# Optimization experiments

Hardware: AMD Instinct MI355X
Metric: run time of the kernel (lower is better)

The kernel has to match this reference:

```python
import jax, jax.numpy as jnp
import numpy as np

N = 32768; D = 384; P = 3; CORR_D = 2 * 49 * P * P  # 882
G_KK = 4096; G_JK = 512
EPS = 1e-3  # LayerNorm eps in the torch module

FLOAT_NAMES = ("net","inp","corr","corr_w1","corr_b1","corr_w2","corr_b2","corr_ln_g","corr_ln_b","corr_w3","corr_b3","norm_g","norm_b","c1_w1","c1_b1","c1_w2","c1_b2","c2_w1","c2_b1","c2_w2","c2_b2","kk_fw","kk_fb","kk_gw","kk_gb","kk_hw","kk_hb","ij_fw","ij_fb","ij_gw","ij_gb","ij_hw","ij_hb","g_ln1_g","g_ln1_b","g1_gw","g1_gb","g1_r1w","g1_r1b","g1_r2w","g1_r2b","g_ln2_g","g_ln2_b","g2_gw","g2_gb","g2_r1w","g2_r1b","g2_r2w","g2_r2b","d_w","d_b","w_w","w_b")

def _ln(x, g, b):
    m = jnp.mean(x, -1, keepdims=True)
    v = jnp.mean((x - m) ** 2, -1, keepdims=True)
    return (x - m) * jax.lax.rsqrt(v + EPS) * g + b

def _mlp2(x, w1, b1, w2, b2):
    return jax.nn.relu(x @ w1 + b1) @ w2 + b2

def _gated_residual(x, gw, gb, r1w, r1b, r2w, r2b):
    gate = jax.nn.sigmoid(x @ gw + gb)
    res = jax.nn.relu(x @ r1w + r1b) @ r2w + r2b
    return x + gate * res

def _soft_agg(x, jx, fw, fb, gw, gb, hw, hb, num_groups):
    # x: [N, D]; jx: [N] group ids -> group-wise softmax weighted sum
    logits = x @ gw + gb
    feats = x @ fw + fb
    gmax = jax.ops.segment_max(logits, jx, num_segments=num_groups)
    e = jnp.exp(logits - gmax[jx])
    den = jax.ops.segment_sum(e, jx, num_segments=num_groups)
    w = e / (den[jx] + 1e-12)
    y = jax.ops.segment_sum(feats * w, jx, num_segments=num_groups)
    return (y @ hw + hb)[jx]

def _forward(p, nix, njx, ukk, ujk):
    # corr encoder MLP
    h = jax.nn.relu(p["corr"] @ p["corr_w1"] + p["corr_b1"]) @ p["corr_w2"] + p["corr_b2"]
    h = jax.nn.relu(_ln(h, p["corr_ln_g"], p["corr_ln_b"])) @ p["corr_w3"] + p["corr_b3"]
    net = p["net"] + p["inp"] + h
    net = _ln(net, p["norm_g"], p["norm_b"])
    mask_ix = (nix >= 0).astype(net.dtype).reshape(1, -1, 1)
    mask_jx = (njx >= 0).astype(net.dtype).reshape(1, -1, 1)
    net = net + _mlp2(mask_ix * net[:, nix], p["c1_w1"], p["c1_b1"], p["c1_w2"], p["c1_b2"])
    net = net + _mlp2(mask_jx * net[:, njx], p["c2_w1"], p["c2_b1"], p["c2_w2"], p["c2_b2"])
    net = net + _soft_agg(net[0], ukk, p["kk_fw"], p["kk_fb"], p["kk_gw"], p["kk_gb"], p["kk_hw"], p["kk_hb"], G_KK)[None]
    net = net + _soft_agg(net[0], ujk, p["ij_fw"], p["ij_fb"], p["ij_gw"], p["ij_gb"], p["ij_hw"], p["ij_hb"], G_JK)[None]
    net = _ln(net, p["g_ln1_g"], p["g_ln1_b"])
    net = _gated_residual(net, p["g1_gw"], p["g1_gb"], p["g1_r1w"], p["g1_r1b"], p["g1_r2w"], p["g1_r2b"])
    net = _ln(net, p["g_ln2_g"], p["g_ln2_b"])
    net = _gated_residual(net, p["g2_gw"], p["g2_gb"], p["g2_r1w"], p["g2_r1b"], p["g2_r2w"], p["g2_r2b"])
    r = jax.nn.relu(net)
    d = r @ p["d_w"] + p["d_b"]               # GradClip is identity in forward
    w = jax.nn.sigmoid(r @ p["w_w"] + p["w_b"])
    return net, d, w

def setup_inputs() -> dict:
    key = jax.random.key(0)
    it = iter(jax.random.split(key, 64))
    def pr(*shape):
        return jax.random.normal(next(it), shape, dtype=jnp.float32) * 0.02
    z = lambda *s: jnp.zeros(s, jnp.float32)
    o = lambda *s: jnp.ones(s, jnp.float32)
    inp = {
        "net": jax.random.normal(next(it), (1, N, D), dtype=jnp.float32),
        "inp": jax.random.normal(next(it), (1, N, D), dtype=jnp.float32),
        "corr": jax.random.normal(next(it), (1, N, CORR_D), dtype=jnp.float32),
        "nix": jax.random.randint(next(it), (N,), 0, N),
        "njx": jax.random.randint(next(it), (N,), 0, N),
        "ukk": jax.random.randint(next(it), (N,), 0, G_KK),
        "ujk": jax.random.randint(next(it), (N,), 0, G_JK),
        "corr_w1": pr(CORR_D, D), "corr_b1": z(D), "corr_w2": pr(D, D), "corr_b2": z(D),
        "corr_ln_g": o(D), "corr_ln_b": z(D), "corr_w3": pr(D, D), "corr_b3": z(D),
        "norm_g": o(D), "norm_b": z(D),
        "c1_w1": pr(D, D), "c1_b1": z(D), "c1_w2": pr(D, D), "c1_b2": z(D),
        "c2_w1": pr(D, D), "c2_b1": z(D), "c2_w2": pr(D, D), "c2_b2": z(D),
        "kk_fw": pr(D, D), "kk_fb": z(D), "kk_gw": pr(D, D), "kk_gb": z(D), "kk_hw": pr(D, D), "kk_hb": z(D),
        "ij_fw": pr(D, D), "ij_fb": z(D), "ij_gw": pr(D, D), "ij_gb": z(D), "ij_hw": pr(D, D), "ij_hb": z(D),
        "g_ln1_g": o(D), "g_ln1_b": z(D),
        "g1_gw": pr(D, D), "g1_gb": z(D), "g1_r1w": pr(D, D), "g1_r1b": z(D), "g1_r2w": pr(D, D), "g1_r2b": z(D),
        "g_ln2_g": o(D), "g_ln2_b": z(D),
        "g2_gw": pr(D, D), "g2_gb": z(D), "g2_r1w": pr(D, D), "g2_r1b": z(D), "g2_r2w": pr(D, D), "g2_r2b": z(D),
        "d_w": pr(D, 2), "d_b": z(2), "w_w": pr(D, 2), "w_b": z(2),
    }
    return inp

def reference(net, inp, corr, corr_w1, corr_b1, corr_w2, corr_b2, corr_ln_g, corr_ln_b, corr_w3, corr_b3, norm_g, norm_b, c1_w1, c1_b1, c1_w2, c1_b2, c2_w1, c2_b1, c2_w2, c2_b2, kk_fw, kk_fb, kk_gw, kk_gb, kk_hw, kk_hb, ij_fw, ij_fb, ij_gw, ij_gb, ij_hw, ij_hb, g_ln1_g, g_ln1_b, g1_gw, g1_gb, g1_r1w, g1_r1b, g1_r2w, g1_r2b, g_ln2_g, g_ln2_b, g2_gw, g2_gb, g2_r1w, g2_r1b, g2_r2w, g2_r2b, d_w, d_b, w_w, w_b, nix, njx, ukk, ujk):
    loc = locals()
    fl = {k: loc[k] for k in FLOAT_NAMES}
    return _forward(fl, nix, njx, ukk, ujk)
```

## Files before the change

### kernel.cpp

```cpp
#include <hip/hip_runtime.h>
#include <hip/hip_bf16.h>
#include <math.h>

#define NR 32768
#define DD 384
#define CDM 882
#define CDMP 896

typedef float f4 __attribute__((ext_vector_type(4)));
typedef float f32x4 __attribute__((ext_vector_type(4)));
typedef __bf16 bf16x8 __attribute__((ext_vector_type(8)));

__device__ inline f4 ld4(const float* p) { f4 v; __builtin_memcpy(&v, p, 16); return v; }
__device__ inline void st4(float* p, f4 v) { __builtin_memcpy(p, &v, 16); }
__device__ inline bf16x8 ld8h(const __bf16* p) { bf16x8 v; __builtin_memcpy(&v, p, 16); return v; }
__device__ inline void st8h(__bf16* p, bf16x8 v) { __builtin_memcpy(p, &v, 16); }

__device__ inline void gl_lds16(const void* g, void* l) {
  __builtin_amdgcn_global_load_lds(
      (const __attribute__((address_space(1))) void*)g,
      (__attribute__((address_space(3))) void*)l, 16, 0, 0);
}

__device__ inline float gred16(float v) {
#pragma unroll
  for (int o = 1; o < 16; o <<= 1) v += __shfl_xor(v, o, 64);
  return v;
}

__global__ __launch_bounds__(256) void corr2bf16_k(const float* __restrict__ src,
                                                   __bf16* __restrict__ dst) {
  int i = blockIdx.x * 256 + threadIdx.x;
  int row = i / 112, c8 = (i - row * 112) * 8;
  const float* sp = src + (size_t)row * CDM + c8;
  bf16x8 h;
  if (c8 + 8 <= CDM) {
#pragma unroll
    for (int e = 0; e < 8; ++e) h[e] = (__bf16)sp[e];
  } else {
#pragma unroll
    for (int e = 0; e < 8; ++e) h[e] = (c8 + e < CDM) ? (__bf16)sp[e] : (__bf16)0.f;
  }
  st8h(dst + (size_t)row * CDMP + c8, h);
}

struct WPtrs { const float* w[19]; };

__global__ __launch_bounds__(256) void trans_all_k(WPtrs P, __bf16* __restrict__ dst) {
  int wi = blockIdx.y;
  const float* W = P.w[wi];
  int i = blockIdx.x * 256 + threadIdx.x;
  if (wi < 18) {
    if (i >= DD * DD) return;
    int n = i / DD, k = i - n * DD;
    dst[(size_t)wi * DD * DD + i] = (__bf16)W[(size_t)k * DD + n];
  } else {
    if (i >= DD * CDMP) return;
    int n = i / CDMP, k = i - n * CDMP;
    dst[(size_t)18 * DD * DD + i] = (k < CDM) ? (__bf16)W[(size_t)k * DD + n] : (__bf16)0.f;
  }
}

struct GP {
  const void* A; const __bf16* WT; const float* bias; __bf16* OUT;
  const __bf16* XRES; const __bf16* GIN;
  const float* p0; const float* p1; const float* p2; const float* p3;
  float* fout; const float* net32; const float* inp32;
  const int* idx; const __bf16* zpage; int M; int K;
};

template <int EPI, int AFP32>
__global__ __launch_bounds__(512, 1) void gemm_k(GP gp) {
  __shared__ __align__(16) __bf16 sm[2 * 32768];
  const int t = threadIdx.x;
  const int w = t >> 6, lane = t & 63;
  const int m0 = blockIdx.x * 128;
  const int fr = lane & 15, fq = lane >> 4;
  const int wr = (w >> 2) * 64, wc = (w & 3) * 96;
  const int K = gp.K;

  const __bf16* aptr[2];
  int aadv[2];
  const __bf16* bptr[6];
#pragma unroll
  for (int j = 0; j < 2; ++j) {
    int rloc = w * 16 + j * 8 + (lane >> 3);
    int cch = (lane & 7) ^ (rloc & 7);
    if constexpr (!AFP32) {
      int ar = gp.idx ? gp.idx[m0 + rloc] : (m0 + rloc);
      if (ar >= 0) { aptr[j] = (const __bf16*)gp.A + (size_t)ar * K + cch * 8; aadv[j] = 64; }
      else { aptr[j] = gp.zpage; aadv[j] = 0; }
    }
  }
#pragma unroll
  for (int j = 0; j < 6; ++j) {
    int rloc = w * 48 + j * 8 + (lane >> 3);
    int cch = (lane & 7) ^ (rloc & 7);
    bptr[j] = gp.WT + (size_t)rloc * K + cch * 8;
  }
  const float* Af = (const float*)gp.A;
  const int NT = K >> 6;

  f32x4 acc[4][6];
#pragma unroll
  for (int a = 0; a < 4; ++a)
#pragma unroll
    for (int b = 0; b < 6; ++b)
#pragma unroll
      for (int j = 0; j < 4; ++j) acc[a][b][j] = 0.f;

  auto stageG = [&](int buf) {
    __bf16* As = sm + buf * 32768;
    __bf16* Bs = As + 8192;
#pragma unroll
    for (int j = 0; j < 2; ++j) {
      gl_lds16(aptr[j], &As[(w * 16 + j * 8) * 64]);
      aptr[j] += aadv[j];
    }
#pragma unroll
    for (int j = 0; j < 6; ++j) {
      gl_lds16(bptr[j], &Bs[(w * 48 + j * 8) * 64]);
      bptr[j] += 64;
    }
  };

  auto stageF = [&](int k0) {
    __bf16* As = sm;
    __bf16* Bs = sm + 8192;
#pragma unroll
    for (int j = 0; j < 2; ++j) {
      int rr = (t >> 3) + 64 * j;
      int cc = t & 7;
      const float* ap = Af + (size_t)(m0 + rr) * K + k0 + cc * 8;
      f4 v0 = ld4(ap), v1 = ld4(ap + 4);
      bf16x8 h;
#pragma unroll
      for (int e = 0; e < 4; ++e) { h[e] = (__bf16)v0[e]; h[4 + e] = (__bf16)v1[e]; }
      *reinterpret_cast<bf16x8*>(&As[rr * 64 + ((cc ^ (rr & 7)) << 3)]) = h;
    }
#pragma unroll
    for (int j = 0; j < 6; ++j) {
      gl_lds16(bptr[j], &Bs[(w * 48 + j * 8) * 64]);
      bptr[j] += 64;
    }
  };

  auto compute = [&](int buf) {
    const __bf16* As = sm + buf * 32768;
    const __bf16* Bs = As + 8192;
#pragma unroll
    for (int kk2 = 0; kk2 < 2; ++kk2) {
      bf16x8 af[4];
      bf16x8 bv[6];
#pragma unroll
      for (int mi = 0; mi < 4; ++mi) {
        int rr = wr + mi * 16 + fr;
        af[mi] = *reinterpret_cast<const bf16x8*>(
            &As[rr * 64 + (((fq + kk2 * 4) ^ (rr & 7)) << 3)]);
      }
#pragma unroll
      for (int ni = 0; ni < 6; ++ni) {
        int rr = wc + ni * 16 + fr;
        bv[ni] = *reinterpret_cast<const bf16x8*>(
            &Bs[rr * 64 + (((fq + kk2 * 4) ^ (rr & 7)) << 3)]);
      }
#pragma unroll
      for (int mi = 0; mi < 4; ++mi)
#pragma unroll
        for (int ni = 0; ni < 6; ++ni)
          acc[mi][ni] = __builtin_amdgcn_mfma_f32_16x16x32_bf16(af[mi], bv[ni],
                                                                acc[mi][ni], 0, 0, 0);
    }
  };

  if constexpr (AFP32) {
    for (int tt = 0; tt < NT; ++tt) {
      if (tt) __syncthreads();
      stageF(tt << 6);
      __syncthreads();
      compute(0);
    }
  } else {
    stageG(0);
    int buf = 0;
    for (int tt = 0; tt < NT; ++tt) {
      if (tt + 1 < NT) {
        stageG(buf ^ 1);
        asm volatile("s_waitcnt vmcnt(8)" ::: "memory");
      } else {
        asm volatile("s_waitcnt vmcnt(0)" ::: "memory");
      }
      __builtin_amdgcn_s_barrier();
      __builtin_amdgcn_sched_barrier(0);
      compute(buf);
      __builtin_amdgcn_s_barrier();
      __builtin_amdgcn_sched_barrier(0);
      buf ^= 1;
    }
  }

  const int nw = w & 3;
  float bcol[6];
#pragma unroll
  for (int ni = 0; ni < 6; ++ni) bcol[ni] = gp.bias[wc + ni * 16 + fr];
#pragma unroll
  for (int mi = 0; mi < 4; ++mi)
#pragma unroll
    for (int ni = 0; ni < 6; ++ni)
#pragma unroll
      for (int j = 0; j < 4; ++j) acc[mi][ni][j] += bcol[ni];

  if constexpr (EPI <= 2) {
#pragma unroll
    for (int mi = 0; mi < 4; ++mi)
#pragma unroll
      for (int ni = 0; ni < 6; ++ni) {
        int col = wc + ni * 16 + fr;
#pragma unroll
        for (int j = 0; j < 4; ++j) {
          int row = m0 + wr + mi * 16 + fq * 4 + j;
          size_t o = (size_t)row * DD + col;
          float v = acc[mi][ni][j];
          if constexpr (EPI == 0) gp.OUT[o] = (__bf16)v;
          else if constexpr (EPI == 1) gp.OUT[o] = (__bf16)fmaxf(v, 0.f);
          else gp.OUT[o] = (__bf16)((float)gp.OUT[o] + v);
        }
      }
  } else {
    if constexpr (EPI == 5) {
#pragma unroll
      for (int mi = 0; mi < 4; ++mi)
#pragma unroll
        for (int ni = 0; ni < 6; ++ni) {
          int col = wc + ni * 16 + fr;
#pragma unroll
          for (int j = 0; j < 4; ++j) {
            int row = m0 + wr + mi * 16 + fq * 4 + j;
            size_t o = (size_t)row * DD + col;
            acc[mi][ni][j] += gp.net32[o] + gp.inp32[o];
          }
        }
    }
    if constexpr (EPI == 6 || EPI == 7) {
#pragma unroll
      for (int mi = 0; mi < 4; ++mi)
#pragma unroll
        for (int ni = 0; ni < 6; ++ni) {
          int col = wc + ni * 16 + fr;
#pragma unroll
          for (int j = 0; j < 4; ++j) {
            int row = m0 + wr + mi * 16 + fq * 4 + j;
            size_t o = (size_t)row * DD + col;
            float gl = (float)gp.GIN[o];
            float sg = 1.f / (1.f + expf(-gl));
            acc[mi][ni][j] = (float)gp.XRES[o] + sg * acc[mi][ni][j];
          }
        }
    }
    __syncthreads();
    if constexpr (EPI != 7) {
      float s1[4][4], s2[4][4];
#pragma unroll
      for (int mi = 0; mi < 4; ++mi)
#pragma unroll
        for (int j = 0; j < 4; ++j) { s1[mi][j] = 0.f; s2[mi][j] = 0.f; }
#pragma unroll
      for (int mi = 0; mi < 4; ++mi)
#pragma unroll
        for (int ni = 0; ni < 6; ++ni)
#pragma unroll
          for (int j = 0; j < 4; ++j) {
            float v = acc[mi][ni][j];
            s1[mi][j] += v;
            s2[mi][j] += v * v;
          }
#pragma unroll
      for (int o = 1; o < 16; o <<= 1)
#pragma unroll
        for (int mi = 0; mi < 4; ++mi)
#pragma unroll
          for (int j = 0; j < 4; ++j) {
            s1[mi][j] += __shfl_xor(s1[mi][j], o, 64);
            s2[mi][j] += __shfl_xor(s2[mi][j], o, 64);
          }
      float* lsum = (float*)sm;
      float* lsq = lsum + 512;
      if (fr == 0) {
#pragma unroll
        for (int mi = 0; mi < 4; ++mi)
#pragma unroll
          for (int j = 0; j < 4; ++j) {
            int rr = wr + mi * 16 + fq * 4 + j;
            lsum[rr * 4 + nw] = s1[mi][j];
            lsq[rr * 4 + nw] = s2[mi][j];
          }
      }
      __syncthreads();
      float mn[4][4], rs[4][4];
#pragma unroll
      for (int mi = 0; mi < 4; ++mi)
#pragma unroll
        for (int j = 0; j < 4; ++j) {
          int rr = wr + mi * 16 + fq * 4 + j;
          float S1 = lsum[rr * 4] + lsum[rr * 4 + 1] + lsum[rr * 4 + 2] + lsum[rr * 4 + 3];
          float S2 = lsq[rr * 4] + lsq[rr * 4 + 1] + lsq[rr * 4 + 2] + lsq[rr * 4 + 3];
          float m = S1 * (1.f / 384.f);
          float va = S2 * (1.f / 384.f) - m * m;
          mn[mi][j] = m;
          rs[mi][j] = rsqrtf(va + 1e-3f);
        }
#pragma unroll
      for (int ni = 0; ni < 6; ++ni) {
        int col = wc + ni * 16 + fr;
        float gg = gp.p0[col], bb = gp.p1[col];
#pragma unroll
        for (int mi = 0; mi < 4; ++mi)
#pragma unroll
          for (int j = 0; j < 4; ++j) {
            int row = m0 + wr + mi * 16 + fq * 4 + j;
            float y = (acc[mi][ni][j] - mn[mi][j]) * rs[mi][j] * gg + bb;
            if constexpr (EPI == 4) y = fmaxf(y, 0.f);
            gp.OUT[(size_t)row * DD + col] = (__bf16)y;
          }
      }
    } else {
      float c0[6], c1[6], c2[6], c3[6];
#pragma unroll
      for (int ni = 0; ni < 6; ++ni) {
        int col = wc + ni * 16 + fr;
        c0[ni] = gp.p0[2 * col];
        c1[ni] = gp.p0[2 * col + 1];
        c2[ni] = gp.p2[2 * col];
        c3[ni] = gp.p2[2 * col + 1];
      }
      float dt[4][4][4];
#pragma unroll
      for (int mi = 0; mi < 4; ++mi)
#pragma unroll
        for (int j = 0; j < 4; ++j)
#pragma unroll
          for (int q = 0; q < 4; ++q) dt[mi][j][q] = 0.f;
#pragma unroll
      for (int mi = 0; mi < 4; ++mi)
#pragma unroll
        for (int ni = 0; ni < 6; ++ni) {
          int col = wc + ni * 16 + fr;
#pragma unroll
          for (int j = 0; j < 4; ++j) {
            int row = m0 + wr + mi * 16 + fq * 4 + j;
            float v = acc[mi][ni][j];
            gp.fout[(size_t)row * DD + col] = v;
            float r = fmaxf(v, 0.f);
            dt[mi][j][0] += r * c0[ni];
            dt[mi][j][1] += r * c1[ni];
            dt[mi][j][2] += r * c2[ni];
            dt[mi][j][3] += r * c3[ni];
          }
        }
#pragma unroll
      for (int o = 1; o < 16; o <<= 1)
#pragma unroll
        for (int mi = 0; mi < 4; ++mi)
#pragma unroll
          for (int j = 0; j < 4; ++j)
#pragma unroll
            for (int q = 0; q < 4; ++q)
              dt[mi][j][q] += __shfl_xor(dt[mi][j][q], o, 64);
      float* lt = (float*)sm;
      if (fr == 0) {
#pragma unroll
        for (int mi = 0; mi < 4; ++mi)
#pragma unroll
          for (int j = 0; j < 4; ++j) {
            int rr = wr + mi * 16 + fq * 4 + j;
#pragma unroll
            for (int q = 0; q < 4; ++q) lt[(rr * 4 + nw) * 4 + q] = dt[mi][j][q];
          }
      }
      __syncthreads();
      if (nw == 0 && fr == 0) {
        float* fd = gp.fout + (size_t)NR * DD;
        float* fw = fd + (size_t)NR * 2;
#pragma unroll
        for (int mi = 0; mi < 4; ++mi)
#pragma unroll
          for (int j = 0; j < 4; ++j) {
            int rr = wr + mi * 16 + fq * 4 + j;
            int row = m0 + rr;
            float T[4];
#pragma unroll
            for (int q = 0; q < 4; ++q)
              T[q] = lt[(rr * 4 + 0) * 4 + q] + lt[(rr * 4 + 1) * 4 + q] +
                     lt[(rr * 4 + 2) * 4 + q] + lt[(rr * 4 + 3) * 4 + q];
            fd[2 * row] = T[0] + gp.p1[0];
            fd[2 * row + 1] = T[1] + gp.p1[1];
            fw[2 * row] = 1.f / (1.f + expf(-(T[2] + gp.p3[0])));
            fw[2 * row + 1] = 1.f / (1.f + expf(-(T[3] + gp.p3[1])));
          }
      }
    }
  }
}

__global__ __launch_bounds__(256) void ln_ag_k(const __bf16* __restrict__ X,
                                               const __bf16* __restrict__ z,
                                               const int* __restrict__ gid,
                                               const float* __restrict__ g,
                                               const float* __restrict__ b,
                                               __bf16* __restrict__ out) {
  int w = threadIdx.x >> 6, lane = threadIdx.x & 63;
  int s = lane & 15, qq = lane >> 4;
  int row = blockIdx.x * 16 + w * 4 + qq;
  int gr = gid[row];
  size_t base = (size_t)row * DD;
  size_t zbase = (size_t)gr * DD;
  float v[24];
#pragma unroll
  for (int i = 0; i < 3; ++i) {
    int col = (s + 16 * i) * 8;
    bf16x8 h = ld8h(X + base + col);
    bf16x8 zz = ld8h(z + zbase + col);
#pragma unroll
    for (int e = 0; e < 8; ++e) v[i * 8 + e] = (float)h[e] + (float)zz[e];
  }
  float sm = 0.f;
#pragma unroll
  for (int i = 0; i < 24; ++i) sm += v[i];
  sm = gred16(sm);
  float mean = sm * (1.f / 384.f);
  float qs = 0.f;
#pragma unroll
  for (int i = 0; i < 24; ++i) { float d = v[i] - mean; qs += d * d; }
  qs = gred16(qs);
  float rs = rsqrtf(qs * (1.f / 384.f) + 1e-3f);
#pragma unroll
  for (int i = 0; i < 3; ++i) {
    int col = (s + 16 * i) * 8;
    f4 g0 = ld4(g + col), g1 = ld4(g + col + 4);
    f4 b0 = ld4(b + col), b1 = ld4(b + col + 4);
    bf16x8 o;
#pragma unroll
    for (int e = 0; e < 4; ++e) {
      o[e] = (__bf16)((v[i * 8 + e] - mean) * rs * g0[e] + b0[e]);
      o[4 + e] = (__bf16)((v[i * 8 + 4 + e] - mean) * rs * g1[e] + b1[e]);
    }
    st8h(out + base + col, o);
  }
}

__global__ __launch_bounds__(256) void hist2_k(const int* __restrict__ ukk,
                                               const int* __restrict__ ujk,
                                               int* __restrict__ ckk,
                                               int* __restrict__ cij) {
  int i = blockIdx.x * 256 + threadIdx.x;
  atomicAdd(&ckk[ukk[i]], 1);
  atomicAdd(&cij[ujk[i]], 1);
}

__device__ inline void scan_body(const int* cnt, int* off, int* curb, int G, int* ls) {
  int t = threadIdx.x;
  int per = G / 256;
  int base = t * per;
  int s = 0;
  for (int i = 0; i < per; ++i) s += cnt[base + i];
  ls[t] = s;
  __syncthreads();
  for (int o = 1; o < 256; o <<= 1) {
    int v = (t >= o) ? ls[t - o] : 0;
    __syncthreads();
    ls[t] += v;
    __syncthreads();
  }
  int run = (t == 0) ? 0 : ls[t - 1];
  for (int i = 0; i < per; ++i) {
    off[base + i] = run;
    run += cnt[base + i];
    curb[base + i] = 0;
  }
  if (t == 255) off[G] = run;
}

__global__ __launch_bounds__(256) void scan2_k(const int* ckk, int* okk, int* qkk,
                                               const int* cij, int* oij, int* qij) {
  __shared__ int ls[256];
  if (blockIdx.x == 0) scan_body(ckk, okk, qkk, 4096, ls);
  else scan_body(cij, oij, qij, 512, ls);
}

__global__ __launch_bounds__(256) void scatter2_k(const int* __restrict__ ukk,
                                                  const int* __restrict__ ujk,
                                                  const int* __restrict__ okk,
                                                  int* __restrict__ qkk,
                                                  int* __restrict__ rkk,
                                                  const int* __restrict__ oij,
                                                  int* __restrict__ qij,
                                                  int* __restrict__ rij) {
  int i = blockIdx.x * 256 + threadIdx.x;
  int g1 = ukk[i];
  rkk[okk[g1] + atomicAdd(&qkk[g1], 1)] = i;
  int g2 = ujk[i];
  rij[oij[g2] + atomicAdd(&qij[g2], 1)] = i;
}

__global__ __launch_bounds__(384) void segagg_k(const __bf16* __restrict__ L,
                                                const __bf16* __restrict__ Ft,
                                                const int* __restrict__ rows,
                                                const int* __restrict__ off,
                                                float* __restrict__ yb) {
  int g = blockIdx.x;
  int c = threadIdx.x;
  int s = off[g], e = off[g + 1];
  float mx = -3.0e38f;
  for (int p = s; p < e; ++p) {
    int r = rows[p];
    mx = fmaxf(mx, (float)L[(size_t)r * DD + c]);
  }
  float num = 0.f, den = 0.f;
  for (int p = s; p < e; ++p) {
    int r = rows[p];
    float lv = (float)L[(size_t)r * DD + c];
    float fv = (float)Ft[(size_t)r * DD + c];
    float ev = expf(lv - mx);
    den += ev;
    num += fv * ev;
  }
  yb[(size_t)g * DD + c] = num / (den + 1e-12f);
}

__global__ __launch_bounds__(256) void addgather_k(__bf16* __restrict__ X,
                                                   const __bf16* __restrict__ z,
                                                   const int* __restrict__ gid) {
  int i = blockIdx.x * 256 + threadIdx.x;
  int row = i / 48, c = (i - row * 48) * 8;
  int g = gid[row];
  size_t lo = (size_t)row * DD + c;
  bf16x8 a = ld8h(X + lo);
  bf16x8 zz = ld8h(z + (size_t)g * DD + c);
  bf16x8 o;
#pragma unroll
  for (int e = 0; e < 8; ++e) o[e] = (__bf16)((float)a[e] + (float)zz[e]);
  st8h(X + lo, o);
}

extern "C" void kernel_launch(void* const* d_in, const int* in_sizes, int n_in,
                              void* d_out, int out_size, void* d_ws, size_t ws_size,
                              hipStream_t stream) {
  const float* in_net = (const float*)d_in[0];
  const float* in_inp = (const float*)d_in[1];
  const float* in_corr = (const float*)d_in[2];
  const int* nix = (const int*)d_in[3];
  const int* njx = (const int*)d_in[4];
  const int* ukk = (const int*)d_in[5];
  const int* ujk = (const int*)d_in[6];
  auto F = [&](int i) { return (const float*)d_in[i]; };

  constexpr size_t MiB = 1024 * 1024;
  constexpr size_t SZ_ACT = (size_t)NR * DD * 2;
  char* ws = (char*)d_ws;
  __bf16* Xc = (__bf16*)(ws);
  __bf16* T2b = (__bf16*)(ws);
  __bf16* Fb = (__bf16*)(ws + SZ_ACT);
  __bf16* zb = (__bf16*)(ws + 2 * SZ_ACT);
  float* yb = (float*)(ws + 2 * SZ_ACT + 3 * MiB);
  __bf16* T1b = (__bf16*)(ws + 60 * MiB);
  char* p = ws + 84 * MiB;
  int* rows_kk = (int*)p; p += (size_t)NR * 4;
  int* rows_ij = (int*)p; p += (size_t)NR * 4;
  int* off_kk = (int*)p; p += 8192 * 4;
  int* off_ij = (int*)p; p += 1024 * 4;
  int* cnt_kk = (int*)p; p += 4096 * 4;
  int* cnt_ij = (int*)p; p += 512 * 4;
  int* curb_kk = (int*)p; p += 4096 * 4;
  int* curb_ij = (int*)p; p += 512 * 4;
  __bf16* wt_all = (__bf16*)p; p += (size_t)18 * DD * DD * 2;
  __bf16* wt_corr1 = (__bf16*)p; p += (size_t)DD * CDMP * 2;
  __bf16* zpage = (__bf16*)p;

  const int widx[18] = {17, 19, 21, 23, 25, 27, 29, 31, 33, 35, 39, 41, 43, 47, 49, 51, 9, 13};
  WPtrs P;
  for (int i = 0; i < 18; ++i) P.w[i] = F(widx[i]);
  P.w[18] = F(7);
  auto WTp = [&](int i) { return wt_all + (size_t)i * DD * DD; };

  hipMemsetAsync(zpage, 0, 256, stream);
  hipMemsetAsync(cnt_kk, 0, 4096 * 4, stream);
  hipMemsetAsync(cnt_ij, 0, 512 * 4, stream);
  trans_all_k<<<dim3(1344, 19), 256, 0, stream>>>(P, wt_all);
  corr2bf16_k<<<NR * 112 / 256, 256, 0, stream>>>(in_corr, Xc);
  hist2_k<<<NR / 256, 256, 0, stream>>>(ukk, ujk, cnt_kk, cnt_ij);
  scan2_k<<<2, 256, 0, stream>>>(cnt_kk, off_kk, curb_kk, cnt_ij, off_ij, curb_ij);
  scatter2_k<<<NR / 256, 256, 0, stream>>>(ukk, ujk, off_kk, curb_kk, rows_kk,
                                           off_ij, curb_ij, rows_ij);

  auto G = [&](int epi, const void* A, const __bf16* WT, const float* bias,
               __bf16* OUT, const __bf16* XRES, const __bf16* GIN,
               const float* p0, const float* p1, const float* p2, const float* p3,
               float* fout, const float* n32, const float* i32,
               const int* idx, int M, int K) {
    GP gp{A, WT, bias, OUT, XRES, GIN, p0, p1, p2, p3, fout, n32, i32, idx, zpage, M, K};
    dim3 g(M / 128), b(512);
    switch (epi) {
      case 0: gemm_k<0, 0><<<g, b, 0, stream>>>(gp); break;
      case 1: gemm_k<1, 0><<<g, b, 0, stream>>>(gp); break;
      case 2: gemm_k<2, 0><<<g, b, 0, stream>>>(gp); break;
      case 4: gemm_k<4, 0><<<g, b, 0, stream>>>(gp); break;
      case 5: gemm_k<5, 0><<<g, b, 0, stream>>>(gp); break;
      case 6: gemm_k<6, 0><<<g, b, 0, stream>>>(gp); break;
      case 7: gemm_k<7, 0><<<g, b, 0, stream>>>(gp); break;
      case 8: gemm_k<0, 1><<<g, b, 0, stream>>>(gp); break;
    }
  };
  auto GS = [&](int epi, const void* A, const __bf16* WT, const float* bias,
                __bf16* OUT, const int* idx, int M, int K) {
    G(epi, A, WT, bias, OUT, nullptr, nullptr, nullptr, nullptr, nullptr, nullptr,
      nullptr, nullptr, nullptr, idx, M, K);
  };

  const int SEGB = NR * 48 / 256;

  GS(1, Xc, wt_corr1, F(8), T1b, nullptr, NR, CDMP);
  G(4, T1b, WTp(16), F(10), T2b, nullptr, nullptr, F(11), F(12), nullptr, nullptr,
    nullptr, nullptr, nullptr, nullptr, NR, DD);
  G(5, T2b, WTp(17), F(14), T1b, nullptr, nullptr, F(15), F(16), nullptr, nullptr,
    nullptr, in_net, in_inp, nullptr, NR, DD);
  GS(1, T1b, WTp(0), F(18), T2b, nix, NR, DD);
  GS(2, T2b, WTp(1), F(20), T1b, nullptr, NR, DD);
  GS(1, T1b, WTp(2), F(22), T2b, njx, NR, DD);
  GS(2, T2b, WTp(3), F(24), T1b, nullptr, NR, DD);
  GS(0, T1b, WTp(5), F(28), T2b, nullptr, NR, DD);
  GS(0, T1b, WTp(4), F(26), Fb, nullptr, NR, DD);
  segagg_k<<<4096, 384, 0, stream>>>(T2b, Fb, rows_kk, off_kk, yb);
  GS(8, yb, WTp(6), F(30), zb, nullptr, 4096, DD);
  addgather_k<<<SEGB, 256, 0, stream>>>(T1b, zb, ukk);
  GS(0, T1b, WTp(8), F(34), T2b, nullptr, NR, DD);
  GS(0, T1b, WTp(7), F(32), Fb, nullptr, NR, DD);
  segagg_k<<<512, 384, 0, stream>>>(T2b, Fb, rows_ij, off_ij, yb);
  GS(8, yb, WTp(9), F(36), zb, nullptr, 512, DD);
  ln_ag_k<<<NR / 16, 256, 0, stream>>>(T1b, zb, ujk, F(37), F(38), T2b);
  GS(0, T2b, WTp(10), F(40), Fb, nullptr, NR, DD);
  GS(1, T2b, WTp(11), F(42), T1b, nullptr, NR, DD);
  G(6, T1b, WTp(12), F(44), T2b, T2b, Fb, F(45), F(46), nullptr, nullptr,
    nullptr, nullptr, nullptr, nullptr, NR, DD);
  GS(0, T2b, WTp(13), F(48), Fb, nullptr, NR, DD);
  GS(1, T2b, WTp(14), F(50), T1b, nullptr, NR, DD);
  G(7, T1b, WTp(15), F(52), nullptr, T2b, Fb, F(53), F(54), F(55), F(56),
    (float*)d_out, nullptr, nullptr, nullptr, NR, DD);
}
```

Measured before the change: 604.5 us.

## Fuse corr bf16 conversion into GEMM and merge shared-input GEMM pairs

Removes the standalone corr fp32-to-bf16 conversion kernel; the first GEMM now loads fp32 corr directly, converts it during staging and handles the K tail with masking. Adds a dual GEMM kernel that loads the shared A row-block into LDS once and runs two weight matrices against it, used for four GEMM pairs. This aims to cut activation reads and kernel launches. In exchange, the dual kernel uses a large LDS footprint and drops the double-buffered B pipeline, and the corr GEMM uses the synchronous fp32 staging path.

Result: no change. 601.2 us, median of 2 (-0.5%).

```diff
diff --git a/kernel.cpp b/kernel.cpp
--- a/kernel.cpp
+++ b/kernel.cpp
@@ -12,7 +12,6 @@
 typedef __bf16 bf16x8 __attribute__((ext_vector_type(8)));
 
 __device__ inline f4 ld4(const float* p) { f4 v; __builtin_memcpy(&v, p, 16); return v; }
-__device__ inline void st4(float* p, f4 v) { __builtin_memcpy(p, &v, 16); }
 __device__ inline bf16x8 ld8h(const __bf16* p) { bf16x8 v; __builtin_memcpy(&v, p, 16); return v; }
 __device__ inline void st8h(__bf16* p, bf16x8 v) { __builtin_memcpy(p, &v, 16); }
 
@@ -26,22 +25,6 @@
 #pragma unroll
   for (int o = 1; o < 16; o <<= 1) v += __shfl_xor(v, o, 64);
   return v;
-}
-
-__global__ __launch_bounds__(256) void corr2bf16_k(const float* __restrict__ src,
-                                                   __bf16* __restrict__ dst) {
-  int i = blockIdx.x * 256 + threadIdx.x;
-  int row = i / 112, c8 = (i - row * 112) * 8;
-  const float* sp = src + (size_t)row * CDM + c8;
-  bf16x8 h;
-  if (c8 + 8 <= CDM) {
-#pragma unroll
-    for (int e = 0; e < 8; ++e) h[e] = (__bf16)sp[e];
-  } else {
-#pragma unroll
-    for (int e = 0; e < 8; ++e) h[e] = (c8 + e < CDM) ? (__bf16)sp[e] : (__bf16)0.f;
-  }
-  st8h(dst + (size_t)row * CDMP + c8, h);
 }
 
 struct WPtrs { const float* w[19]; };
@@ -66,8 +49,253 @@
   const __bf16* XRES; const __bf16* GIN;
   const float* p0; const float* p1; const float* p2; const float* p3;
   float* fout; const float* net32; const float* inp32;
-  const int* idx; const __bf16* zpage; int M; int K;
+  const int* idx; const __bf16* zpage; int M; int K; int Kr;
 };
+
+__device__ __forceinline__ void mfma_block(const __bf16* As, const __bf16* Bs,
+                                           f32x4 (&acc)[4][6], int wr, int wc,
+                                           int fr, int fq) {
+#pragma unroll
+  for (int kk2 = 0; kk2 < 2; ++kk2) {
+    bf16x8 af[4];
+    bf16x8 bv[6];
+#pragma unroll
+    for (int mi = 0; mi < 4; ++mi) {
+      int rr = wr + mi * 16 + fr;
+      af[mi] = *reinterpret_cast<const bf16x8*>(
+          &As[rr * 64 + (((fq + kk2 * 4) ^ (rr & 7)) << 3)]);
+    }
+#pragma unroll
+    for (int ni = 0; ni < 6; ++ni) {
+      int rr = wc + ni * 16 + fr;
+      bv[ni] = *reinterpret_cast<const bf16x8*>(
+          &Bs[rr * 64 + (((fq + kk2 * 4) ^ (rr & 7)) << 3)]);
+    }
+#pragma unroll
+    for (int mi = 0; mi < 4; ++mi)
+#pragma unroll
+      for (int ni = 0; ni < 6; ++ni)
+        acc[mi][ni] = __builtin_amdgcn_mfma_f32_16x16x32_bf16(af[mi], bv[ni],
+                                                              acc[mi][ni], 0, 0, 0);
+  }
+}
+
+__device__ __forceinline__ void zero_acc(f32x4 (&acc)[4][6]) {
+#pragma unroll
+  for (int a = 0; a < 4; ++a)
+#pragma unroll
+    for (int b = 0; b < 6; ++b)
+#pragma unroll
+      for (int j = 0; j < 4; ++j) acc[a][b][j] = 0.f;
+}
+
+template <int EPI>
+__device__ __forceinline__ void epilogue(const GP& gp, f32x4 (&acc)[4][6],
+                                         __bf16* sm, int m0, int w, int lane) {
+  const int fr = lane & 15, fq = lane >> 4;
+  const int wr = (w >> 2) * 64, wc = (w & 3) * 96;
+  const int nw = w & 3;
+  float bcol[6];
+#pragma unroll
+  for (int ni = 0; ni < 6; ++ni) bcol[ni] = gp.bias[wc + ni * 16 + fr];
+#pragma unroll
+  for (int mi = 0; mi < 4; ++mi)
+#pragma unroll
+    for (int ni = 0; ni < 6; ++ni)
+#pragma unroll
+      for (int j = 0; j < 4; ++j) acc[mi][ni][j] += bcol[ni];
+
+  if constexpr (EPI <= 2) {
+#pragma unroll
+    for (int mi = 0; mi < 4; ++mi)
+#pragma unroll
+      for (int ni = 0; ni < 6; ++ni) {
+        int col = wc + ni * 16 + fr;
+#pragma unroll
+        for (int j = 0; j < 4; ++j) {
+          int row = m0 + wr + mi * 16 + fq * 4 + j;
+          size_t o = (size_t)row * DD + col;
+          float v = acc[mi][ni][j];
+          if constexpr (EPI == 0) gp.OUT[o] = (__bf16)v;
+          else if constexpr (EPI == 1) gp.OUT[o] = (__bf16)fmaxf(v, 0.f);
+          else gp.OUT[o] = (__bf16)((float)gp.OUT[o] + v);
+        }
+      }
+  } else {
+    if constexpr (EPI == 5) {
+#pragma unroll
+      for (int mi = 0; mi < 4; ++mi)
+#pragma unroll
+        for (int ni = 0; ni < 6; ++ni) {
+          int col = wc + ni * 16 + fr;
+#pragma unroll
+          for (int j = 0; j < 4; ++j) {
+            int row = m0 + wr + mi * 16 + fq * 4 + j;
+            size_t o = (size_t)row * DD + col;
+            acc[mi][ni][j] += gp.net32[o] + gp.inp32[o];
+          }
+        }
+    }
+    if constexpr (EPI == 6 || EPI == 7) {
+#pragma unroll
+      for (int mi = 0; mi < 4; ++mi)
+#pragma unroll
+        for (int ni = 0; ni < 6; ++ni) {
+          int col = wc + ni * 16 + fr;
+#pragma unroll
+          for (int j = 0; j < 4; ++j) {
+            int row = m0 + wr + mi * 16 + fq * 4 + j;
+            size_t o = (size_t)row * DD + col;
+            float gl = (float)gp.GIN[o];
+            float sg = 1.f / (1.f + expf(-gl));
+            acc[mi][ni][j] = (float)gp.XRES[o] + sg * acc[mi][ni][j];
+          }
+        }
+    }
+    __syncthreads();
+    if constexpr (EPI != 7) {
+      float s1[4][4], s2[4][4];
+#pragma unroll
+      for (int mi = 0; mi < 4; ++mi)
+#pragma unroll
+        for (int j = 0; j < 4; ++j) { s1[mi][j] = 0.f; s2[mi][j] = 0.f; }
+#pragma unroll
+      for (int mi = 0; mi < 4; ++mi)
+#pragma unroll
+        for (int ni = 0; ni < 6; ++ni)
+#pragma unroll
+          for (int j = 0; j < 4; ++j) {
+            float v = acc[mi][ni][j];
+            s1[mi][j] += v;
+            s2[mi][j] += v * v;
+          }
+#pragma unroll
+      for (int o = 1; o < 16; o <<= 1)
+#pragma unroll
+        for (int mi = 0; mi < 4; ++mi)
+#pragma unroll
+          for (int j = 0; j < 4; ++j) {
+            s1[mi][j] += __shfl_xor(s1[mi][j], o, 64);
+            s2[mi][j] += __shfl_xor(s2[mi][j], o, 64);
+          }
+      float* lsum = (float*)sm;
+      float* lsq = lsum + 512;
+      if (fr == 0) {
+#pragma unroll
+        for (int mi = 0; mi < 4; ++mi)
+#pragma unroll
+          for (int j = 0; j < 4; ++j) {
+            int rr = wr + mi * 16 + fq * 4 + j;
+            lsum[rr * 4 + nw] = s1[mi][j];
+            lsq[rr * 4 + nw] = s2[mi][j];
+          }
+      }
+      __syncthreads();
+      float mn[4][4], rs[4][4];
+#pragma unroll
+      for (int mi = 0; mi < 4; ++mi)
+#pragma unroll
+        for (int j = 0; j < 4; ++j) {
+          int rr = wr + mi * 16 + fq * 4 + j;
+          float S1 = lsum[rr * 4] + lsum[rr * 4 + 1] + lsum[rr * 4 + 2] + lsum[rr * 4 + 3];
+          float S2 = lsq[rr * 4] + lsq[rr * 4 + 1] + lsq[rr * 4 + 2] + lsq[rr * 4 + 3];
+          float m = S1 * (1.f / 384.f);
+          float va = S2 * (1.f / 384.f) - m * m;
+          mn[mi][j] = m;
+          rs[mi][j] = rsqrtf(va + 1e-3f);
+        }
+#pragma unroll
+      for (int ni = 0; ni < 6; ++ni) {
+        int col = wc + ni * 16 + fr;
+        float gg = gp.p0[col], bb = gp.p1[col];
+#pragma unroll
+        for (int mi = 0; mi < 4; ++mi)
+#pragma unroll
+          for (int j = 0; j < 4; ++j) {
+            int row = m0 + wr + mi * 16 + fq * 4 + j;
+            float y = (acc[mi][ni][j] - mn[mi][j]) * rs[mi][j] * gg + bb;
+            if constexpr (EPI == 4) y = fmaxf(y, 0.f);
+            gp.OUT[(size_t)row * DD + col] = (__bf16)y;
+          }
+      }
+    } else {
+      float c0[6], c1[6], c2[6], c3[6];
+#pragma unroll
+      for (int ni = 0; ni < 6; ++ni) {
+        int col = wc + ni * 16 + fr;
+        c0[ni] = gp.p0[2 * col];
+        c1[ni] = gp.p0[2 * col + 1];
+        c2[ni] = gp.p2[2 * col];
+        c3[ni] = gp.p2[2 * col + 1];
+      }
+      float dt[4][4][4];
+#pragma unroll
+      for (int mi = 0; mi < 4; ++mi)
+#pragma unroll
+        for (int j = 0; j < 4; ++j)
+#pragma unroll
+          for (int q = 0; q < 4; ++q) dt[mi][j][q] = 0.f;
+#pragma unroll
+      for (int mi = 0; mi < 4; ++mi)
+#pragma unroll
+        for (int ni = 0; ni < 6; ++ni) {
+          int col = wc + ni * 16 + fr;
+#pragma unroll
+          for (int j = 0; j < 4; ++j) {
+            int row = m0 + wr + mi * 16 + fq * 4 + j;
+            float v = acc[mi][ni][j];
+            gp.fout[(size_t)row * DD + col] = v;
+            float r = fmaxf(v, 0.f);
+            dt[mi][j][0] += r * c0[ni];
+            dt[mi][j][1] += r * c1[ni];
+            dt[mi][j][2] += r * c2[ni];
+            dt[mi][j][3] += r * c3[ni];
+          }
+        }
+#pragma unroll
+      for (int o = 1; o < 16; o <<= 1)
+#pragma unroll
+        for (int mi = 0; mi < 4; ++mi)
+#pragma unroll
+          for (int j = 0; j < 4; ++j)
+#pragma unroll
+            for (int q = 0; q < 4; ++q)
+              dt[mi][j][q] += __shfl_xor(dt[mi][j][q], o, 64);
+      float* lt = (float*)sm;
+      if (fr == 0) {
+#pragma unroll
+        for (int mi = 0; mi < 4; ++mi)
+#pragma unroll
+          for (int j = 0; j < 4; ++j) {
+            int rr = wr + mi * 16 + fq * 4 + j;
+#pragma unroll
+            for (int q = 0; q < 4; ++q) lt[(rr * 4 + nw) * 4 + q] = dt[mi][j][q];
+          }
+      }
+      __syncthreads();
+      if (nw == 0 && fr == 0) {
+        float* fd = gp.fout + (size_t)NR * DD;
+        float* fw = fd + (size_t)NR * 2;
+#pragma unroll
+        for (int mi = 0; mi < 4; ++mi)
+#pragma unroll
+          for (int j = 0; j < 4; ++j) {
+            int rr = wr + mi * 16 + fq * 4 + j;
+            int row = m0 + rr;
+            float T[4];
+#pragma unroll
+            for (int q = 0; q < 4; ++q)
+              T[q] = lt[(rr * 4 + 0) * 4 + q] + lt[(rr * 4 + 1) * 4 + q] +
+                     lt[(rr * 4 + 2) * 4 + q] + lt[(rr * 4 + 3) * 4 + q];
+            fd[2 * row] = T[0] + gp.p1[0];
+            fd[2 * row + 1] = T[1] + gp.p1[1];
+            fw[2 * row] = 1.f / (1.f + expf(-(T[2] + gp.p3[0])));
+            fw[2 * row + 1] = 1.f / (1.f + expf(-(T[3] + gp.p3[1])));
+          }
+      }
+    }
+  }
+}
 
 template <int EPI, int AFP32>
 __global__ __launch_bounds__(512, 1) void gemm_k(GP gp) {
@@ -99,15 +327,11 @@
     bptr[j] = gp.WT + (size_t)rloc * K + cch * 8;
   }
   const float* Af = (const float*)gp.A;
+  const int Kr = gp.Kr;
   const int NT = K >> 6;
 
   f32x4 acc[4][6];
-#pragma unroll
-  for (int a = 0; a < 4; ++a)
-#pragma unroll
-    for (int b = 0; b < 6; ++b)
-#pragma unroll
-      for (int j = 0; j < 4; ++j) acc[a][b][j] = 0.f;
+  zero_acc(acc);
 
   auto stageG = [&](int buf) {
     __bf16* As = sm + buf * 32768;
@@ -131,45 +355,23 @@
     for (int j = 0; j < 2; ++j) {
       int rr = (t >> 3) + 64 * j;
       int cc = t & 7;
-      const float* ap = Af + (size_t)(m0 + rr) * K + k0 + cc * 8;
-      f4 v0 = ld4(ap), v1 = ld4(ap + 4);
+      int kb = k0 + cc * 8;
+      const float* ap = Af + (size_t)(m0 + rr) * Kr + kb;
       bf16x8 h;
-#pragma unroll
-      for (int e = 0; e < 4; ++e) { h[e] = (__bf16)v0[e]; h[4 + e] = (__bf16)v1[e]; }
+      if (kb + 8 <= Kr) {
+        f4 v0 = ld4(ap), v1 = ld4(ap + 4);
+#pragma unroll
+        for (int e = 0; e < 4; ++e) { h[e] = (__bf16)v0[e]; h[4 + e] = (__bf16)v1[e]; }
+      } else {
+#pragma unroll
+        for (int e = 0; e < 8; ++e) h[e] = (kb + e < Kr) ? (__bf16)ap[e] : (__bf16)0.f;
+      }
       *reinterpret_cast<bf16x8*>(&As[rr * 64 + ((cc ^ (rr & 7)) << 3)]) = h;
     }
 #pragma unroll
     for (int j = 0; j < 6; ++j) {
       gl_lds16(bptr[j], &Bs[(w * 48 + j * 8) * 64]);
       bptr[j] += 64;
-    }
-  };
-
-  auto compute = [&](int buf) {
-    const __bf16* As = sm + buf * 32768;
-    const __bf16* Bs = As + 8192;
-#pragma unroll
-    for (int kk2 = 0; kk2 < 2; ++kk2) {
-      bf16x8 af[4];
-      bf16x8 bv[6];
-#pragma unroll
-      for (int mi = 0; mi < 4; ++mi) {
-        int rr = wr + mi * 16 + fr;
-        af[mi] = *reinterpret_cast<const bf16x8*>(
-            &As[rr * 64 + (((fq + kk2 * 4) ^ (rr & 7)) << 3)]);
-      }
-#pragma unroll
-      for (int ni = 0; ni < 6; ++ni) {
-        int rr = wc + ni * 16 + fr;
-        bv[ni] = *reinterpret_cast<const bf16x8*>(
-            &Bs[rr * 64 + (((fq + kk2 * 4) ^ (rr & 7)) << 3)]);
-      }
-#pragma unroll
-      for (int mi = 0; mi < 4; ++mi)
-#pragma unroll
-        for (int ni = 0; ni < 6; ++ni)
-          acc[mi][ni] = __builtin_amdgcn_mfma_f32_16x16x32_bf16(af[mi], bv[ni],
-                                                                acc[mi][ni], 0, 0, 0);
     }
   };
 
@@ -178,7 +380,7 @@
       if (tt) __syncthreads();
       stageF(tt << 6);
       __syncthreads();
-      compute(0);
+      mfma_block(sm, sm + 8192, acc, wr, wc, fr, fq);
     }
   } else {
     stageG(0);
@@ -192,214 +394,72 @@
       }
       __builtin_amdgcn_s_barrier();
       __builtin_amdgcn_sched_barrier(0);
-      compute(buf);
+      mfma_block(sm + buf * 32768, sm + buf * 32768 + 8192, acc, wr, wc, fr, fq);
       __builtin_amdgcn_s_barrier();
       __builtin_amdgcn_sched_barrier(0);
       buf ^= 1;
     }
   }
-
-  const int nw = w & 3;
-  float bcol[6];
-#pragma unroll
-  for (int ni = 0; ni < 6; ++ni) bcol[ni] = gp.bias[wc + ni * 16 + fr];
-#pragma unroll
-  for (int mi = 0; mi < 4; ++mi)
-#pragma unroll
-    for (int ni = 0; ni < 6; ++ni)
-#pragma unroll
-      for (int j = 0; j < 4; ++j) acc[mi][ni][j] += bcol[ni];
-
-  if constexpr (EPI <= 2) {
-#pragma unroll
-    for (int mi = 0; mi < 4; ++mi)
-#pragma unroll
-      for (int ni = 0; ni < 6; ++ni) {
-        int col = wc + ni * 16 + fr;
-#pragma unroll
-        for (int j = 0; j < 4; ++j) {
-          int row = m0 + wr + mi * 16 + fq * 4 + j;
-          size_t o = (size_t)row * DD + col;
-          float v = acc[mi][ni][j];
-          if constexpr (EPI == 0) gp.OUT[o] = (__bf16)v;
-          else if constexpr (EPI == 1) gp.OUT[o] = (__bf16)fmaxf(v, 0.f);
-          else gp.OUT[o] = (__bf16)((float)gp.OUT[o] + v);
-        }
-      }
-  } else {
-    if constexpr (EPI == 5) {
-#pragma unroll
-      for (int mi = 0; mi < 4; ++mi)
-#pragma unroll
-        for (int ni = 0; ni < 6; ++ni) {
-          int col = wc + ni * 16 + fr;
-#pragma unroll
-          for (int j = 0; j < 4; ++j) {
-            int row = m0 + wr + mi * 16 + fq * 4 + j;
-            size_t o = (size_t)row * DD + col;
-            acc[mi][ni][j] += gp.net32[o] + gp.inp32[o];
-          }
-        }
-    }
-    if constexpr (EPI == 6 || EPI == 7) {
-#pragma unroll
-      for (int mi = 0; mi < 4; ++mi)
-#pragma unroll
-        for (int ni = 0; ni < 6; ++ni) {
-          int col = wc + ni * 16 + fr;
-#pragma unroll
-          for (int j = 0; j < 4; ++j) {
-            int row = m0 + wr + mi * 16 + fq * 4 + j;
-            size_t o = (size_t)row * DD + col;
-            float gl = (float)gp.GIN[o];
-            float sg = 1.f / (1.f + expf(-gl));
-            acc[mi][ni][j] = (float)gp.XRES[o] + sg * acc[mi][ni][j];
-          }
-        }
-    }
-    __syncthreads();
-    if constexpr (EPI != 7) {
-      float s1[4][4], s2[4][4];
-#pragma unroll
-      for (int mi = 0; mi < 4; ++mi)
-#pragma unroll
-        for (int j = 0; j < 4; ++j) { s1[mi][j] = 0.f; s2[mi][j] = 0.f; }
-#pragma unroll
-      for (int mi = 0; mi < 4; ++mi)
-#pragma unroll
-        for (int ni = 0; ni < 6; ++ni)
-#pragma unroll
-          for (int j = 0; j < 4; ++j) {
-            float v = acc[mi][ni][j];
-            s1[mi][j] += v;
-            s2[mi][j] += v * v;
-          }
-#pragma unroll
-      for (int o = 1; o < 16; o <<= 1)
-#pragma unroll
-        for (int mi = 0; mi < 4; ++mi)
-#pragma unroll
-          for (int j = 0; j < 4; ++j) {
-            s1[mi][j] += __shfl_xor(s1[mi][j], o, 64);
-            s2[mi][j] += __shfl_xor(s2[mi][j], o, 64);
-          }
-      float* lsum = (float*)sm;
-      float* lsq = lsum + 512;
-      if (fr == 0) {
-#pragma unroll
-        for (int mi = 0; mi < 4; ++mi)
-#pragma unroll
-          for (int j = 0; j < 4; ++j) {
-            int rr = wr + mi * 16 + fq * 4 + j;
-            lsum[rr * 4 + nw] = s1[mi][j];
-            lsq[rr * 4 + nw] = s2[mi][j];
-          }
-      }
+  epilogue<EPI>(gp, acc, sm, m0, w, lane);
+}
+
+template <int EPIA, int EPIB>
+__global__ __launch_bounds__(512, 1) void gemm_dual_k(GP ga, GP gb) {
+  __shared__ __align__(16) __bf16 sm[73728];
+  const int t = threadIdx.x;
+  const int w = t >> 6, lane = t & 63;
+  const int m0 = blockIdx.x * 128;
+  const int fr = lane & 15, fq = lane >> 4;
+  const int wr = (w >> 2) * 64, wc = (w & 3) * 96;
+  __bf16* As = sm;
+  __bf16* Bs = sm + 49152;
+
+  {
+    const __bf16* aptr[2];
+#pragma unroll
+    for (int j = 0; j < 2; ++j) {
+      int rloc = w * 16 + j * 8 + (lane >> 3);
+      int cch = (lane & 7) ^ (rloc & 7);
+      aptr[j] = (const __bf16*)ga.A + (size_t)(m0 + rloc) * DD + cch * 8;
+    }
+#pragma unroll
+    for (int tt = 0; tt < 6; ++tt)
+#pragma unroll
+      for (int j = 0; j < 2; ++j) {
+        gl_lds16(aptr[j], &As[tt * 8192 + (w * 16 + j * 8) * 64]);
+        aptr[j] += 64;
+      }
+  }
+
+  f32x4 acc[4][6];
+  auto run_phase = [&](const GP& gp) {
+    const __bf16* bptr[6];
+#pragma unroll
+    for (int j = 0; j < 6; ++j) {
+      int rloc = w * 48 + j * 8 + (lane >> 3);
+      int cch = (lane & 7) ^ (rloc & 7);
+      bptr[j] = gp.WT + (size_t)rloc * DD + cch * 8;
+    }
+    for (int tt = 0; tt < 6; ++tt) {
       __syncthreads();
-      float mn[4][4], rs[4][4];
-#pragma unroll
-      for (int mi = 0; mi < 4; ++mi)
-#pragma unroll
-        for (int j = 0; j < 4; ++j) {
-          int rr = wr + mi * 16 + fq * 4 + j;
-          float S1 = lsum[rr * 4] + lsum[rr * 4 + 1] + lsum[rr * 4 + 2] + lsum[rr * 4 + 3];
-          float S2 = lsq[rr * 4] + lsq[rr * 4 + 1] + lsq[rr * 4 + 2] + lsq[rr * 4 + 3];
-          float m = S1 * (1.f / 384.f);
-          float va = S2 * (1.f / 384.f) - m * m;
-          mn[mi][j] = m;
-          rs[mi][j] = rsqrtf(va + 1e-3f);
-        }
-#pragma unroll
-      for (int ni = 0; ni < 6; ++ni) {
-        int col = wc + ni * 16 + fr;
-        float gg = gp.p0[col], bb = gp.p1[col];
-#pragma unroll
-        for (int mi = 0; mi < 4; ++mi)
-#pragma unroll
-          for (int j = 0; j < 4; ++j) {
-            int row = m0 + wr + mi * 16 + fq * 4 + j;
-            float y = (acc[mi][ni][j] - mn[mi][j]) * rs[mi][j] * gg + bb;
-            if constexpr (EPI == 4) y = fmaxf(y, 0.f);
-            gp.OUT[(size_t)row * DD + col] = (__bf16)y;
-          }
-      }
-    } else {
-      float c0[6], c1[6], c2[6], c3[6];
-#pragma unroll
-      for (int ni = 0; ni < 6; ++ni) {
-        int col = wc + ni * 16 + fr;
-        c0[ni] = gp.p0[2 * col];
-        c1[ni] = gp.p0[2 * col + 1];
-        c2[ni] = gp.p2[2 * col];
-        c3[ni] = gp.p2[2 * col + 1];
-      }
-      float dt[4][4][4];
-#pragma unroll
-      for (int mi = 0; mi < 4; ++mi)
-#pragma unroll
-        for (int j = 0; j < 4; ++j)
-#pragma unroll
-          for (int q = 0; q < 4; ++q) dt[mi][j][q] = 0.f;
-#pragma unroll
-      for (int mi = 0; mi < 4; ++mi)
-#pragma unroll
-        for (int ni = 0; ni < 6; ++ni) {
-          int col = wc + ni * 16 + fr;
-#pragma unroll
-          for (int j = 0; j < 4; ++j) {
-            int row = m0 + wr + mi * 16 + fq * 4 + j;
-            float v = acc[mi][ni][j];
-            gp.fout[(size_t)row * DD + col] = v;
-            float r = fmaxf(v, 0.f);
-            dt[mi][j][0] += r * c0[ni];
-            dt[mi][j][1] += r * c1[ni];
-            dt[mi][j][2] += r * c2[ni];
-            dt[mi][j][3] += r * c3[ni];
-          }
-        }
-#pragma unroll
-      for (int o = 1; o < 16; o <<= 1)
-#pragma unroll
-        for (int mi = 0; mi < 4; ++mi)
-#pragma unroll
-          for (int j = 0; j < 4; ++j)
-#pragma unroll
-            for (int q = 0; q < 4; ++q)
-              dt[mi][j][q] += __shfl_xor(dt[mi][j][q], o, 64);
-      float* lt = (float*)sm;
-      if (fr == 0) {
-#pragma unroll
-        for (int mi = 0; mi < 4; ++mi)
-#pragma unroll
-          for (int j = 0; j < 4; ++j) {
-            int rr = wr + mi * 16 + fq * 4 + j;
-#pragma unroll
-            for (int q = 0; q < 4; ++q) lt[(rr * 4 + nw) * 4 + q] = dt[mi][j][q];
-          }
-      }
-      __syncthreads();
-      if (nw == 0 && fr == 0) {
-        float* fd = gp.fout + (size_t)NR * DD;
-        float* fw = fd + (size_t)NR * 2;
-#pragma unroll
-        for (int mi = 0; mi < 4; ++mi)
-#pragma unroll
-          for (int j = 0; j < 4; ++j) {
-            int rr = wr + mi * 16 + fq * 4 + j;
-            int row = m0 + rr;
-            float T[4];
-#pragma unroll
-            for (int q = 0; q < 4; ++q)
-              T[q] = lt[(rr * 4 + 0) * 4 + q] + lt[(rr * 4 + 1) * 4 + q] +
-                     lt[(rr * 4 + 2) * 4 + q] + lt[(rr * 4 + 3) * 4 + q];
-            fd[2 * row] = T[0] + gp.p1[0];
-            fd[2 * row + 1] = T[1] + gp.p1[1];
-            fw[2 * row] = 1.f / (1.f + expf(-(T[2] + gp.p3[0])));
-            fw[2 * row + 1] = 1.f / (1.f + expf(-(T[3] + gp.p3[1])));
-          }
-      }
-    }
-  }
+#pragma unroll
+      for (int j = 0; j < 6; ++j) {
+        gl_lds16(bptr[j], &Bs[(w * 48 + j * 8) * 64]);
+        bptr[j] += 64;
+      }
+      asm volatile("s_waitcnt vmcnt(0)" ::: "memory");
+      __builtin_amdgcn_s_barrier();
+      __builtin_amdgcn_sched_barrier(0);
+      mfma_block(As + tt * 8192, Bs, acc, wr, wc, fr, fq);
+    }
+  };
+
+  zero_acc(acc);
+  run_phase(ga);
+  epilogue<EPIA>(ga, acc, sm + 49152 + 24576, m0, w, lane);
+  zero_acc(acc);
+  run_phase(gb);
+  epilogue<EPIB>(gb, acc, sm + 49152 + 24576, m0, w, lane);
 }
 
 __global__ __launch_bounds__(256) void ln_ag_k(const __bf16* __restrict__ X,
@@ -557,7 +617,6 @@
   constexpr size_t MiB = 1024 * 1024;
   constexpr size_t SZ_ACT = (size_t)NR * DD * 2;
   char* ws = (char*)d_ws;
-  __bf16* Xc = (__bf16*)(ws);
   __bf16* T2b = (__bf16*)(ws);
   __bf16* Fb = (__bf16*)(ws + SZ_ACT);
   __bf16* zb = (__bf16*)(ws + 2 * SZ_ACT);
@@ -586,7 +645,6 @@
   hipMemsetAsync(cnt_kk, 0, 4096 * 4, stream);
   hipMemsetAsync(cnt_ij, 0, 512 * 4, stream);
   trans_all_k<<<dim3(1344, 19), 256, 0, stream>>>(P, wt_all);
-  corr2bf16_k<<<NR * 112 / 256, 256, 0, stream>>>(in_corr, Xc);
   hist2_k<<<NR / 256, 256, 0, stream>>>(ukk, ujk, cnt_kk, cnt_ij);
   scan2_k<<<2, 256, 0, stream>>>(cnt_kk, off_kk, curb_kk, cnt_ij, off_ij, curb_ij);
   scatter2_k<<<NR / 256, 256, 0, stream>>>(ukk, ujk, off_kk, curb_kk, rows_kk,
@@ -596,8 +654,8 @@
                __bf16* OUT, const __bf16* XRES, const __bf16* GIN,
                const float* p0, const float* p1, const float* p2, const float* p3,
                float* fout, const float* n32, const float* i32,
-               const int* idx, int M, int K) {
-    GP gp{A, WT, bias, OUT, XRES, GIN, p0, p1, p2, p3, fout, n32, i32, idx, zpage, M, K};
+               const int* idx, int M, int K, int Kr) {
+    GP gp{A, WT, bias, OUT, XRES, GIN, p0, p1, p2, p3, fout, n32, i32, idx, zpage, M, K, Kr};
     dim3 g(M / 128), b(512);
     switch (epi) {
       case 0: gemm_k<0, 0><<<g, b, 0, stream>>>(gp); break;
@@ -608,41 +666,49 @@
       case 6: gemm_k<6, 0><<<g, b, 0, stream>>>(gp); break;
       case 7: gemm_k<7, 0><<<g, b, 0, stream>>>(gp); break;
       case 8: gemm_k<0, 1><<<g, b, 0, stream>>>(gp); break;
+      case 9: gemm_k<1, 1><<<g, b, 0, stream>>>(gp); break;
     }
   };
   auto GS = [&](int epi, const void* A, const __bf16* WT, const float* bias,
                 __bf16* OUT, const int* idx, int M, int K) {
     G(epi, A, WT, bias, OUT, nullptr, nullptr, nullptr, nullptr, nullptr, nullptr,
-      nullptr, nullptr, nullptr, idx, M, K);
+      nullptr, nullptr, nullptr, idx, M, K, K);
   };
+  auto GD = [&](const void* A, const __bf16* WTa, const float* ba, __bf16* Oa,
+                const __bf16* WTb, const float* bb, __bf16* Ob, int epib) {
+    GP ga{A, WTa, ba, Oa, nullptr, nullptr, nullptr, nullptr, nullptr, nullptr,
+          nullptr, nullptr, nullptr, nullptr, zpage, NR, DD, DD};
+    GP gb{A, WTb, bb, Ob, nullptr, nullptr, nullptr, nullptr, nullptr, nullptr,
+          nullptr, nullptr, nullptr, nullptr, zpage, NR, DD, DD};
+    dim3 g(NR / 128), b(512);
+    if (epib == 0) gemm_dual_k<0, 0><<<g, b, 0, stream>>>(ga, gb);
+    else gemm_dual_k<0, 1><<<g, b, 0, stream>>>(ga, gb);
+  };
 
   const int SEGB = NR * 48 / 256;
 
-  GS(1, Xc, wt_corr1, F(8), T1b, nullptr, NR, CDMP);
+  G(9, in_corr, wt_corr1, F(8), T1b, nullptr, nullptr, nullptr, nullptr, nullptr,
+    nullptr, nullptr, nullptr, nullptr, nullptr, NR, CDMP, CDM);
   G(4, T1b, WTp(16), F(10), T2b, nullptr, nullptr, F(11), F(12), nullptr, nullptr,
-    nullptr, nullptr, nullptr, nullptr, NR, DD);
+    nullptr, nullptr, nullptr, nullptr, NR, DD, DD);
   G(5, T2b, WTp(17), F(14), T1b, nullptr, nullptr, F(15), F(16), nullptr, nullptr,
-    nullptr, in_net, in_inp, nullptr, NR, DD);
+    nullptr, in_net, in_inp, nullptr, NR, DD, DD);
   GS(1, T1b, WTp(0), F(18), T2b, nix, NR, DD);
   GS(2, T2b, WTp(1), F(20), T1b, nullptr, NR, DD);
   GS(1, T1b, WTp(2), F(22), T2b, njx, NR, DD);
   GS(2, T2b, WTp(3), F(24), T1b, nullptr, NR, DD);
-  GS(0, T1b, WTp(5), F(28), T2b, nullptr, NR, DD);
-  GS(0, T1b, WTp(4), F(26), Fb, nullptr, NR, DD);
+  GD(T1b, WTp(5), F(28), T2b, WTp(4), F(26), Fb, 0);
   segagg_k<<<4096, 384, 0, stream>>>(T2b, Fb, rows_kk, off_kk, yb);
   GS(8, yb, WTp(6), F(30), zb, nullptr, 4096, DD);
   addgather_k<<<SEGB, 256, 0, stream>>>(T1b, zb, ukk);
-  GS(0, T1b, WTp(8), F(34), T2b, nullptr, NR, DD);
-  GS(0, T1b, WTp(7), F(32), Fb, nullptr, NR, DD);
+  GD(T1b, WTp(8), F(34), T2b, WTp(7), F(32), Fb, 0);
   segagg_k<<<512, 384, 0, stream>>>(T2b, Fb, rows_ij, off_ij, yb);
   GS(8, yb, WTp(9), F(36), zb, nullptr, 512, DD);
   ln_ag_k<<<NR / 16, 256, 0, stream>>>(T1b, zb, ujk, F(37), F(38), T2b);
-  GS(0, T2b, WTp(10), F(40), Fb, nullptr, NR, DD);
-  GS(1, T2b, WTp(11), F(42), T1b, nullptr, NR, DD);
+  GD(T2b, WTp(10), F(40), Fb, WTp(11), F(42), T1b, 1);
   G(6, T1b, WTp(12), F(44), T2b, T2b, Fb, F(45), F(46), nullptr, nullptr,
-    nullptr, nullptr, nullptr, nullptr, NR, DD);
-  GS(0, T2b, WTp(13), F(48), Fb, nullptr, NR, DD);
-  GS(1, T2b, WTp(14), F(50), T1b, nullptr, NR, DD);
+    nullptr, nullptr, nullptr, nullptr, NR, DD, DD);
+  GD(T2b, WTp(13), F(48), Fb, WTp(14), F(50), T1b, 1);
   G(7, T1b, WTp(15), F(52), nullptr, T2b, Fb, F(53), F(54), F(55), F(56),
-    (float*)d_out, nullptr, nullptr, nullptr, NR, DD);
-}
+    (float*)d_out, nullptr, nullptr, nullptr, NR, DD, DD);
+}
```
